# Kernel optimization log

Measured on AMD Instinct MI355X. Metric: run time of the kernel, lower is better.

Reference implementation:

```python
import jax, jax.numpy as jnp
from jax import lax
import numpy as np

DIM = 768
HEADS = 12
HD = DIM // HEADS  # 64
STRIDE = (1, 2, 2)
KER = (3, 3, 3)
PAD = [(1, 1), (1, 1), (1, 1)]
EPS = 1e-5


def _layernorm(x, g, b):
    mu = jnp.mean(x, axis=-1, keepdims=True)
    var = jnp.var(x, axis=-1, keepdims=True)
    return (x - mu) * lax.rsqrt(var + EPS) * g + b


def _attention_pool(t, wconv, g, b, T, H, W):
    # t: [B, heads, 1 + T*H*W, HD]; depthwise conv3d pooling on non-cls tokens
    B, Nh, _, Cd = t.shape
    cls_tok = t[:, :, :1, :]
    body = t[:, :, 1:, :].reshape(B * Nh, T, H, W, Cd).transpose(0, 4, 1, 2, 3)  # [BN, C, T, H, W]
    body = lax.conv_general_dilated(
        body, wconv, window_strides=STRIDE, padding=PAD,
        feature_group_count=Cd,
        dimension_numbers=('NCDHW', 'OIDHW', 'NCDHW'))
    Tp, Hp, Wp = body.shape[2], body.shape[3], body.shape[4]
    body = body.reshape(B, Nh, Cd, Tp * Hp * Wp).transpose(0, 1, 3, 2)  # [B, heads, Lp, C]
    t = jnp.concatenate([cls_tok, body], axis=2)
    t = _layernorm(t, g, b)
    return t, (Tp, Hp, Wp)


def setup_inputs() -> dict:
    key = jax.random.key(0)
    ks = jax.random.split(key, 12)
    T, H, W = 8, 28, 28
    B = 4
    N = 1 + T * H * W  # cls + thw tokens = 6273
    s = 0.02
    inp = {
        'x': jax.random.normal(ks[0], (B, N, DIM), jnp.float32),
        'qkv_w': jax.random.normal(ks[1], (DIM, 3 * DIM), jnp.float32) * s,
        'qkv_b': jnp.zeros((3 * DIM,), jnp.float32),
        'proj_w': jax.random.normal(ks[2], (DIM, DIM), jnp.float32) * s,
        'proj_b': jnp.zeros((DIM,), jnp.float32),
        'wq': jax.random.normal(ks[3], (HD, 1, 3, 3, 3), jnp.float32) * s,
        'wk': jax.random.normal(ks[4], (HD, 1, 3, 3, 3), jnp.float32) * s,
        'wv': jax.random.normal(ks[5], (HD, 1, 3, 3, 3), jnp.float32) * s,
        'gq': jnp.ones((HD,), jnp.float32), 'bq': jnp.zeros((HD,), jnp.float32),
        'gk': jnp.ones((HD,), jnp.float32), 'bk': jnp.zeros((HD,), jnp.float32),
        'gv': jnp.ones((HD,), jnp.float32), 'bv': jnp.zeros((HD,), jnp.float32),
        'thw_t': T, 'thw_h': H, 'thw_w': W,
    }
    return inp


def reference(x, qkv_w, qkv_b, proj_w, proj_b, wq, wk, wv,
              gq, bq, gk, bk, gv, bv, thw_t, thw_h, thw_w):
    B, N, C = x.shape
    scale = HD ** -0.5
    qkv = (x @ qkv_w + qkv_b).reshape(B, N, 3, HEADS, HD).transpose(2, 0, 3, 1, 4)
    q, k, v = qkv[0], qkv[1], qkv[2]  # [B, heads, N, HD]
    q, q_shape = _attention_pool(q, wq, gq, bq, thw_t, thw_h, thw_w)
    k, _ = _attention_pool(k, wk, gk, bk, thw_t, thw_h, thw_w)
    v, _ = _attention_pool(v, wv, gv, bv, thw_t, thw_h, thw_w)
    attn = jax.nn.softmax(jnp.einsum('bhqd,bhkd->bhqk', q, k) * scale, axis=-1)
    Nq = q.shape[2]
    out = jnp.einsum('bhqk,bhkd->bhqd', attn, v).transpose(0, 2, 1, 3).reshape(B, Nq, C)
    out = out @ proj_w + proj_b
    return out
```

## Files before the change

### kernel.cpp

```cpp
#include <hip/hip_runtime.h>
#include <hip/hip_bf16.h>

#define BB      4
#define NTOK    6273
#define NPOOL   1569
#define NPOOLP  1600
#define NHEADS  12
#define TT      8
#define HH      28
#define WW      28
#define HP      14
#define WP      14

typedef __attribute__((ext_vector_type(8))) _Float16 f16x8;
typedef __attribute__((ext_vector_type(4))) float f32x4;
typedef unsigned short u16;

#define AS1(p) ((const __attribute__((address_space(1))) void*)(p))
#define AS3(p) ((__attribute__((address_space(3))) void*)(p))

static __device__ __forceinline__ u16 f2h(float x) {
    union { _Float16 h; u16 u; } c; c.h = (_Float16)x; return c.u;
}
static __device__ __forceinline__ float h2f(u16 u) {
    union { u16 u; _Float16 h; } c; c.u = u; return (float)c.h;
}

__global__ __launch_bounds__(256) void cvt_f32_f16_kernel(
    const float* __restrict__ in, u16* __restrict__ out, int n4)
{
    int i = blockIdx.x * 256 + threadIdx.x;
    const int stride = gridDim.x * 256;
    for (; i < n4; i += stride) {
        const float4 v = ((const float4*)in)[i];
        ushort4 o;
        o.x = f2h(v.x); o.y = f2h(v.y); o.z = f2h(v.z); o.w = f2h(v.w);
        ((ushort4*)out)[i] = o;
    }
}

__global__ __launch_bounds__(256) void transpose_cvt_kernel(
    const float* __restrict__ W, u16* __restrict__ t, int K, int N)
{
    __shared__ float tile[32][33];
    const int n0 = blockIdx.x * 32, k0 = blockIdx.y * 32;
    const int tx = threadIdx.x, ty = threadIdx.y;
    #pragma unroll
    for (int i = 0; i < 4; ++i)
        tile[ty + i * 8][tx] = W[(size_t)(k0 + ty + i * 8) * N + n0 + tx];
    __syncthreads();
    #pragma unroll
    for (int i = 0; i < 4; ++i) {
        const int n = n0 + ty + i * 8;
        t[(size_t)n * K + k0 + tx] = f2h(tile[tx][ty + i * 8]);
    }
}

__global__ __launch_bounds__(256) void wt_transpose_kernel(
    const float* __restrict__ wq, const float* __restrict__ wk,
    const float* __restrict__ wv, u16* __restrict__ wTh)
{
    const int which = blockIdx.x;
    const float* w = (which == 0) ? wq : (which == 1) ? wk : wv;
    u16* o = wTh + which * 27 * 64;
    for (int i = threadIdx.x; i < 27 * 64; i += 256) {
        const int j = i >> 6, d = i & 63;
        o[j * 64 + d] = f2h(w[d * 27 + j]);
    }
}

#define GBK 64
#define GNKT 12

__global__ __launch_bounds__(512, 2) void gemm256_qkv_kernel(
    const u16* __restrict__ Af, const u16* __restrict__ Bt,
    const float* __restrict__ bias, int M,
    u16* __restrict__ o0, u16* __restrict__ o1, u16* __restrict__ o2)
{
    __shared__ __align__(16) u16 A_s[4][128 * 64];
    __shared__ __align__(16) u16 B_s[4][128 * 64];

    const int tid  = threadIdx.x;
    const int lane = tid & 63;
    const int w    = tid >> 6;
    const int wr   = w >> 2;
    const int wc   = w & 3;

    const int nwg = gridDim.x;
    const int qch = nwg >> 3, rch = nwg & 7;
    const int xcd = blockIdx.x & 7, idx = blockIdx.x >> 3;
    const int wg  = (xcd < rch ? xcd * (qch + 1) : rch * (qch + 1) + (xcd - rch) * qch) + idx;
    const int m0 = (wg / 9) * 256;
    const int nb = wg % 9;
    const int n0 = nb * 256;

    const int srow = tid >> 3;
    const int scc  = ((tid & 7) ^ (srow & 7)) * 8;
    unsigned offA[2][2], offB[2][2];
    #pragma unroll
    for (int h = 0; h < 2; ++h)
        #pragma unroll
        for (int i = 0; i < 2; ++i) {
            offA[h][i] = (unsigned)(min(m0 + h * 128 + i * 64 + srow, M - 1) * 768 + scc);
            offB[h][i] = (unsigned)((n0 + h * 128 + i * 64 + srow) * 768 + scc);
        }

#define STGA(slot, h, tt) do { \
    __builtin_amdgcn_global_load_lds(AS1(Af + offA[h][0] + (tt) * 64), AS3(&A_s[slot][w * 512]), 16, 0, 0); \
    __builtin_amdgcn_global_load_lds(AS1(Af + offA[h][1] + (tt) * 64), AS3(&A_s[slot][4096 + w * 512]), 16, 0, 0); \
} while (0)
#define STGB(slot, h, tt) do { \
    __builtin_amdgcn_global_load_lds(AS1(Bt + offB[h][0] + (tt) * 64), AS3(&B_s[slot][w * 512]), 16, 0, 0); \
    __builtin_amdgcn_global_load_lds(AS1(Bt + offB[h][1] + (tt) * 64), AS3(&B_s[slot][4096 + w * 512]), 16, 0, 0); \
} while (0)

    STGA(0, 0, 0); STGB(0, 0, 0); STGA(1, 1, 0); STGB(1, 1, 0);
    STGA(2, 0, 1); STGB(2, 0, 1); STGA(3, 1, 1);
    asm volatile("s_waitcnt vmcnt(6)" ::: "memory");
    __builtin_amdgcn_s_barrier();

    f32x4 acc[8][4] = {};
    const int fr = lane & 15, fq = lane >> 4;
    const int ck0 = (fq ^ (fr & 7)) * 8;
    const int ck1 = ((4 + fq) ^ (fr & 7)) * 8;
    const int arow = fr * 64;
    const int brow = (wc & 1) * 4096 + fr * 64;

    for (int it = 0; it < GNKT / 2; ++it) {
        #pragma unroll
        for (int par = 0; par < 2; ++par) {
            const int t  = it * 2 + par;
            const int sa = par ? 2 + wr : wr;
            const int sb = par ? 2 + (wc >> 1) : (wc >> 1);

            f16x8 aF[4][2], aG[4][2], bLo[2][2], bHi[2][2];

            if (t < GNKT - 1) STGB(par ? 1 : 3, 1, t + 1);
            #pragma unroll
            for (int m = 0; m < 4; ++m)
                #pragma unroll
                for (int kh = 0; kh < 2; ++kh)
                    aF[m][kh] = *(const f16x8*)&A_s[sa][m * 1024 + arow + (kh ? ck1 : ck0)];
            #pragma unroll
            for (int n = 0; n < 2; ++n)
                #pragma unroll
                for (int kh = 0; kh < 2; ++kh)
                    bLo[n][kh] = *(const f16x8*)&B_s[sb][brow + n * 1024 + (kh ? ck1 : ck0)];
            __builtin_amdgcn_s_setprio(1);
            #pragma unroll
            for (int m = 0; m < 4; ++m)
                #pragma unroll
                for (int n = 0; n < 2; ++n) {
                    acc[m][n] = __builtin_amdgcn_mfma_f32_16x16x32_f16(aF[m][0], bLo[n][0], acc[m][n], 0, 0, 0);
                    acc[m][n] = __builtin_amdgcn_mfma_f32_16x16x32_f16(aF[m][1], bLo[n][1], acc[m][n], 0, 0, 0);
                }
            __builtin_amdgcn_s_setprio(0);
            __builtin_amdgcn_s_barrier();

            #pragma unroll
            for (int n = 0; n < 2; ++n)
                #pragma unroll
                for (int kh = 0; kh < 2; ++kh)
                    bHi[n][kh] = *(const f16x8*)&B_s[sb][brow + (n + 2) * 1024 + (kh ? ck1 : ck0)];
            __builtin_amdgcn_s_setprio(1);
            #pragma unroll
            for (int m = 0; m < 4; ++m)
                #pragma unroll
                for (int n = 0; n < 2; ++n) {
                    acc[m][n + 2] = __builtin_amdgcn_mfma_f32_16x16x32_f16(aF[m][0], bHi[n][0], acc[m][n + 2], 0, 0, 0);
                    acc[m][n + 2] = __builtin_amdgcn_mfma_f32_16x16x32_f16(aF[m][1], bHi[n][1], acc[m][n + 2], 0, 0, 0);
                }
            __builtin_amdgcn_s_setprio(0);
            __builtin_amdgcn_s_barrier();

            if (t < GNKT - 2) STGB(par ? 2 : 0, 0, t + 2);
            #pragma unroll
            for (int m = 0; m < 4; ++m)
                #pragma unroll
                for (int kh = 0; kh < 2; ++kh)
                    aG[m][kh] = *(const f16x8*)&A_s[sa][(m + 4) * 1024 + arow + (kh ? ck1 : ck0)];
            __builtin_amdgcn_s_setprio(1);
            #pragma unroll
            for (int m = 0; m < 4; ++m)
                #pragma unroll
                for (int n = 0; n < 2; ++n) {
                    acc[m + 4][n + 2] = __builtin_amdgcn_mfma_f32_16x16x32_f16(aG[m][0], bHi[n][0], acc[m + 4][n + 2], 0, 0, 0);
                    acc[m + 4][n + 2] = __builtin_amdgcn_mfma_f32_16x16x32_f16(aG[m][1], bHi[n][1], acc[m + 4][n + 2], 0, 0, 0);
                }
            __builtin_amdgcn_s_setprio(0);
            __builtin_amdgcn_s_barrier();

            if (t < GNKT - 2) { STGA(par ? 2 : 0, 0, t + 2); STGA(par ? 3 : 1, 1, t + 2); }
            __builtin_amdgcn_s_setprio(1);
            #pragma unroll
            for (int m = 0; m < 4; ++m)
                #pragma unroll
                for (int n = 0; n < 2; ++n) {
                    acc[m + 4][n] = __builtin_amdgcn_mfma_f32_16x16x32_f16(aG[m][0], bLo[n][0], acc[m + 4][n], 0, 0, 0);
                    acc[m + 4][n] = __builtin_amdgcn_mfma_f32_16x16x32_f16(aG[m][1], bLo[n][1], acc[m + 4][n], 0, 0, 0);
                }
            __builtin_amdgcn_s_setprio(0);
            if (t < GNKT - 2) asm volatile("s_waitcnt vmcnt(6)" ::: "memory");
            else              asm volatile("s_waitcnt vmcnt(0)" ::: "memory");
            __builtin_amdgcn_s_barrier();
        }
    }
#undef STGA
#undef STGB

    const int s = nb / 3;
    u16* const dsts = (s == 0) ? o0 : (s == 1) ? o1 : o2;
    #pragma unroll
    for (int m = 0; m < 8; ++m) {
        const int growb = m0 + wr * 128 + m * 16 + fq * 4;
        #pragma unroll
        for (int j = 0; j < 4; ++j) {
            const int grow = growb + j;
            if (grow >= M) continue;
            const int bidx = grow / NTOK;
            const int ntok = grow - bidx * NTOK;
            #pragma unroll
            for (int n = 0; n < 4; ++n) {
                const int gcol = n0 + wc * 64 + n * 16 + fr;
                const float v = acc[m][n][j] + bias[gcol];
                const int rem = gcol - s * 768;
                const int h = rem >> 6, d = rem & 63;
                dsts[(size_t)((bidx * NHEADS + h) * NTOK + ntok) * 64 + d] = f2h(v);
            }
        }
    }
}

template<int NBLK, bool QKV, typename OutT>
__global__ __launch_bounds__(512) void gemm_fp16_kernel(
    const u16* __restrict__ Af, const u16* __restrict__ Bt,
    const float* __restrict__ bias, int M,
    OutT* __restrict__ o0, OutT* __restrict__ o1, OutT* __restrict__ o2)
{
    __shared__ __align__(16) u16 A_s[128 * 32];
    __shared__ __align__(16) u16 B_s[128 * 32];

    const int tid  = threadIdx.x;
    const int lane = tid & 63;
    const int w    = tid >> 6;
    const int wr   = w >> 2, wc = w & 3;

    const int nwg = gridDim.x;
    const int qch = nwg >> 3, rch = nwg & 7;
    const int xcd = blockIdx.x & 7, idx = blockIdx.x >> 3;
    const int wg  = (xcd < rch ? xcd * (qch + 1) : rch * (qch + 1) + (xcd - rch) * qch) + idx;
    const int m0 = (wg / NBLK) * 128;
    const int n0 = (wg % NBLK) * 128;

    f32x4 acc[4][2] = {};

    const int srow   = lane >> 2;
    const int sslot  = (lane & 3) ^ ((srow >> 1) & 3);

    for (int kt = 0; kt < 24; ++kt) {
        const int k0 = kt * 32;
        __syncthreads();

        {
            const int rb = w * 16;
            const int ra = min(m0 + rb + srow, M - 1);
            __builtin_amdgcn_global_load_lds(AS1(Af + (size_t)ra * 768 + k0 + sslot * 8),
                                             AS3(&A_s[rb * 32]), 16, 0, 0);
            __builtin_amdgcn_global_load_lds(AS1(Bt + (size_t)(n0 + rb + srow) * 768 + k0 + sslot * 8),
                                             AS3(&B_s[rb * 32]), 16, 0, 0);
        }
        __syncthreads();

        const int fr = lane & 15, fq = lane >> 4;
        const int rslot = (fq ^ ((fr >> 1) & 3)) << 3;
        f16x8 a[4], b[2];
        #pragma unroll
        for (int m = 0; m < 4; ++m)
            a[m] = *(const f16x8*)&A_s[(wr * 64 + m * 16 + fr) * 32 + rslot];
        #pragma unroll
        for (int n = 0; n < 2; ++n)
            b[n] = *(const f16x8*)&B_s[(wc * 32 + n * 16 + fr) * 32 + rslot];

        #pragma unroll
        for (int m = 0; m < 4; ++m)
            #pragma unroll
            for (int n = 0; n < 2; ++n)
                acc[m][n] = __builtin_amdgcn_mfma_f32_16x16x32_f16(a[m], b[n], acc[m][n], 0, 0, 0);
    }

    const int fr = lane & 15, fq = lane >> 4;
    #pragma unroll
    for (int m = 0; m < 4; ++m) {
        const int grow_base = m0 + wr * 64 + m * 16 + fq * 4;
        #pragma unroll
        for (int j = 0; j < 4; ++j) {
            const int grow = grow_base + j;
            if (grow >= M) continue;
            int b = 0, ntok = 0;
            if (QKV) { b = grow / NTOK; ntok = grow - b * NTOK; }
            #pragma unroll
            for (int n = 0; n < 2; ++n) {
                const int gcol = n0 + wc * 32 + n * 16 + fr;
                const float v = acc[m][n][j] + bias[gcol];
                if (QKV) {
                    const int s = gcol / 768;
                    const int rem = gcol - s * 768;
                    const int h = rem >> 6, d = rem & 63;
                    OutT* dst = (s == 0) ? o0 : (s == 1) ? o1 : o2;
                    dst[(size_t)((b * NHEADS + h) * NTOK + ntok) * 64 + d] = (OutT)f2h(v);
                } else {
                    o0[(size_t)grow * (NBLK * 128) + gcol] = (OutT)v;
                }
            }
        }
    }
}

#define PL_PG  50
#define PL_NWG (3 * 48 * PL_PG)
__global__ __launch_bounds__(256) void pool_ln_kernel(
    const u16* __restrict__ qr, const u16* __restrict__ kr, const u16* __restrict__ vr,
    const u16* __restrict__ wTh,
    const float* __restrict__ gq, const float* __restrict__ bq,
    const float* __restrict__ gk, const float* __restrict__ bk,
    const float* __restrict__ gv, const float* __restrict__ bv,
    u16* __restrict__ qph, u16* __restrict__ kph, u16* __restrict__ vpt)
{
    const int wg = (blockIdx.x & 7) * (PL_NWG / 8) + (blockIdx.x >> 3);
    const int which = wg / (48 * PL_PG);
    const int rem   = wg - which * (48 * PL_PG);
    const int bh    = rem / PL_PG;
    const int pg    = rem - bh * PL_PG;
    const int wv_   = threadIdx.x >> 6;
    const int lane  = threadIdx.x & 63;
    const int tg    = lane >> 3;
    const int d0    = (lane & 7) * 8;

    const int p  = pg * 32 + wv_ * 8 + tg;
    const int pc = min(p, NPOOL - 1);

    const u16*   in  = (which == 0) ? qr : (which == 1) ? kr : vr;
    const u16*   wTb = wTh + which * 27 * 64;
    const float* g   = (which == 0) ? gq : (which == 1) ? gk : gv;
    const float* bb_ = (which == 0) ? bq : (which == 1) ? bk : bv;
    const float qscale = (which == 0) ? 0.125f : 1.0f;

    const size_t inb = (size_t)bh * NTOK * 64;

    float s[8] = {};
    if (pc == 0) {
        const f16x8 t = *(const f16x8*)&in[inb + d0];
        #pragma unroll
        for (int c = 0; c < 8; ++c) s[c] = (float)t[c];
    } else {
        const int idx = pc - 1;
        const int tp = idx / (HP * WP);
        const int r2 = idx - tp * (HP * WP);
        const int hp = r2 / WP;
        const int wp = r2 - hp * WP;

        const f16x8 z8 = (f16x8)(_Float16)0.0f;
        #pragma unroll
        for (int kt = 0; kt < 3; ++kt) {
            const int it = tp + kt - 1;
            #pragma unroll
            for (int kh = 0; kh < 3; ++kh) {
                const int ih = hp * 2 + kh - 1;
                #pragma unroll
                for (int kw = 0; kw < 3; ++kw) {
                    const int iw = wp * 2 + kw - 1;
                    const int j  = kt * 9 + kh * 3 + kw;
                    const bool ok = (it >= 0) & (it < TT) & (ih >= 0) & (ih < HH) &
                                    (iw >= 0) & (iw < WW);
                    const int n   = 1 + (it * HH + ih) * WW + iw;
                    const int n_c = ok ? n : 0;
                    const f16x8 tv  = *(const f16x8*)&in[inb + (size_t)n_c * 64 + d0];
                    const f16x8 wv8 = *(const f16x8*)&wTb[j * 64 + d0];
                    const f16x8 ts  = ok ? tv : z8;
                    #pragma unroll
                    for (int c = 0; c < 8; ++c)
                        s[c] = fmaf((float)wv8[c], (float)ts[c], s[c]);
                }
            }
        }
    }

    float sum = 0.f, ssq = 0.f;
    #pragma unroll
    for (int c = 0; c < 8; ++c) { sum += s[c]; ssq += s[c] * s[c]; }
    #pragma unroll
    for (int off = 1; off < 8; off <<= 1) {
        sum += __shfl_xor(sum, off);
        ssq += __shfl_xor(ssq, off);
    }
    const float mu  = sum * (1.f / 64.f);
    const float var = ssq * (1.f / 64.f) - mu * mu;
    const float rs  = rsqrtf(var + 1e-5f);

    float g8[8], b8[8];
    {
        const float4 g0 = *(const float4*)&g[d0];
        const float4 g1 = *(const float4*)&g[d0 + 4];
        const float4 b0 = *(const float4*)&bb_[d0];
        const float4 b1 = *(const float4*)&bb_[d0 + 4];
        g8[0]=g0.x; g8[1]=g0.y; g8[2]=g0.z; g8[3]=g0.w;
        g8[4]=g1.x; g8[5]=g1.y; g8[6]=g1.z; g8[7]=g1.w;
        b8[0]=b0.x; b8[1]=b0.y; b8[2]=b0.z; b8[3]=b0.w;
        b8[4]=b1.x; b8[5]=b1.y; b8[6]=b1.z; b8[7]=b1.w;
    }

    u16 oo[8];
    #pragma unroll
    for (int c = 0; c < 8; ++c)
        oo[c] = f2h(((s[c] - mu) * rs * g8[c] + b8[c]) * qscale);

    if (which == 2) {
        u16* base = vpt + (size_t)bh * 64 * NPOOLP + p;
        if (p < NPOOL) {
            #pragma unroll
            for (int c = 0; c < 8; ++c)
                base[(size_t)(d0 + c) * NPOOLP] = oo[c];
        } else {
            #pragma unroll
            for (int c = 0; c < 8; ++c)
                base[(size_t)(d0 + c) * NPOOLP] = 0;
        }
    } else if (p < NPOOL) {
        u16* out = (which == 0) ? qph : kph;
        u16* dst = &out[((size_t)bh * NPOOL + p) * 64 + d0];
        *(ushort4*)&dst[0] = *(ushort4*)&oo[0];
        *(ushort4*)&dst[4] = *(ushort4*)&oo[4];
    }
}

__global__ __launch_bounds__(256) void flash_attn_fp16_kernel(
    const u16* __restrict__ qh, const u16* __restrict__ kh,
    const u16* __restrict__ vt, float* __restrict__ accf,
    float* __restrict__ lf)
{
    __shared__ __align__(16) u16 K_s[64 * 64];
    __shared__ __align__(16) u16 V_s[64 * 64];
    __shared__ __align__(16) u16 P_s[4][32 * 64];

    const int bh = blockIdx.y;
    const int q0 = blockIdx.x * 128;
    const int z  = blockIdx.z;
    const int kt_lo = z ? 13 : 0, kt_hi = z ? 25 : 13;
    const int tid = threadIdx.x;
    const int w = tid >> 6, lane = tid & 63;
    const int fr = lane & 15, fq = lane >> 4;
    const int l8 = lane >> 3;
    const int sw = 8 * ((lane & 7) ^ l8);

    const size_t hb  = (size_t)bh * NPOOL * 64;
    const size_t vtb = (size_t)bh * 64 * NPOOLP;
    float* accb = accf + (size_t)z * BB * NPOOL * 768;
    float* lb   = lf   + (size_t)z * 48 * NPOOL;

    f16x8 qf_[2][2];
    #pragma unroll
    for (int qf = 0; qf < 2; ++qf) {
        const int row = min(q0 + w * 32 + qf * 16 + fr, NPOOL - 1);
        #pragma unroll
        for (int half = 0; half < 2; ++half)
            qf_[qf][half] = *(const f16x8*)&qh[hb + (size_t)row * 64 + half * 32 + fq * 8];
    }

    f16x8 ones;
    #pragma unroll
    for (int i = 0; i < 8; ++i) ones[i] = (_Float16)1.0f;

    f32x4 acc[2][4] = {};
    f32x4 l_acc[2] = {};

    #define LDSW(buf, row, colbyte) \
        (*(const f16x8*)((const char*)(buf) + ((row) * 128 + ((colbyte) ^ (((row) & 7) << 4)))))

    for (int kt = kt_lo; kt < kt_hi; ++kt) {
        const int k0 = kt * 64;
        __syncthreads();

        #pragma unroll
        for (int i = 0; i < 2; ++i) {
            const int rb = w * 16 + i * 8;
            const int r  = rb + l8;
            const int gk = min(k0 + r, NPOOL - 1);
            __builtin_amdgcn_global_load_lds(AS1(kh + hb + (size_t)gk * 64 + sw),
                                             AS3(&K_s[rb * 64]), 16, 0, 0);
            __builtin_amdgcn_global_load_lds(AS1(vt + vtb + (size_t)r * NPOOLP + k0 + sw),
                                             AS3(&V_s[rb * 64]), 16, 0, 0);
        }
        __syncthreads();

        f32x4 sv[2][4];
        #pragma unroll
        for (int nf = 0; nf < 4; ++nf) {
            const int krow = nf * 16 + fr;
            const f16x8 kf0 = LDSW(K_s, krow, fq * 16);
            const f16x8 kf1 = LDSW(K_s, krow, 64 + fq * 16);
            #pragma unroll
            for (int qf = 0; qf < 2; ++qf) {
                f32x4 s = {};
                s = __builtin_amdgcn_mfma_f32_16x16x32_f16(qf_[qf][0], kf0, s, 0, 0, 0);
                s = __builtin_amdgcn_mfma_f32_16x16x32_f16(qf_[qf][1], kf1, s, 0, 0, 0);
                sv[qf][nf] = s;
            }
        }

        #pragma unroll
        for (int nf = 0; nf < 4; ++nf) {
            const bool valid = (k0 + nf * 16 + fr) < NPOOL;
            #pragma unroll
            for (int qf = 0; qf < 2; ++qf) {
                #pragma unroll
                for (int j = 0; j < 4; ++j) {
                    const float p = valid ? __expf(sv[qf][nf][j]) : 0.f;
                    const int row = qf * 16 + fq * 4 + j;
                    const int bo  = row * 128 + ((nf * 32 + fr * 2) ^ ((row & 7) << 4));
                    *(u16*)((char*)&P_s[w][0] + bo) = f2h(p);
                }
            }
        }
        __builtin_amdgcn_sched_barrier(0);

        f16x8 pa[2][2];
        #pragma unroll
        for (int qf = 0; qf < 2; ++qf) {
            const int prow = qf * 16 + fr;
            pa[qf][0] = LDSW(&P_s[w][0], prow, fq * 16);
            pa[qf][1] = LDSW(&P_s[w][0], prow, 64 + fq * 16);
            l_acc[qf] = __builtin_amdgcn_mfma_f32_16x16x32_f16(pa[qf][0], ones, l_acc[qf], 0, 0, 0);
            l_acc[qf] = __builtin_amdgcn_mfma_f32_16x16x32_f16(pa[qf][1], ones, l_acc[qf], 0, 0, 0);
        }
        #pragma unroll
        for (int df = 0; df < 4; ++df) {
            const int vrow = df * 16 + fr;
            const f16x8 v0 = LDSW(V_s, vrow, fq * 16);
            const f16x8 v1 = LDSW(V_s, vrow, 64 + fq * 16);
            acc[0][df] = __builtin_amdgcn_mfma_f32_16x16x32_f16(pa[0][0], v0, acc[0][df], 0, 0, 0);
            acc[0][df] = __builtin_amdgcn_mfma_f32_16x16x32_f16(pa[0][1], v1, acc[0][df], 0, 0, 0);
            acc[1][df] = __builtin_amdgcn_mfma_f32_16x16x32_f16(pa[1][0], v0, acc[1][df], 0, 0, 0);
            acc[1][df] = __builtin_amdgcn_mfma_f32_16x16x32_f16(pa[1][1], v1, acc[1][df], 0, 0, 0);
        }
    }
    #undef LDSW

    const int b = bh / NHEADS, h = bh % NHEADS;
    #pragma unroll
    for (int qf = 0; qf < 2; ++qf) {
        #pragma unroll
        for (int j = 0; j < 4; ++j) {
            const int q = q0 + w * 32 + qf * 16 + fq * 4 + j;
            if (q >= NPOOL) continue;
            float* dst = &accb[((size_t)b * NPOOL + q) * 768 + h * 64];
            #pragma unroll
            for (int df = 0; df < 4; ++df)
                dst[df * 16 + fr] = acc[qf][df][j];
            if (fr == 0)
                lb[(size_t)bh * NPOOL + q] = l_acc[qf][j];
        }
    }
}

__global__ __launch_bounds__(256) void combine_kernel(
    const float* __restrict__ acc0, const float* __restrict__ acc1,
    const float* __restrict__ l0, const float* __restrict__ l1,
    u16* __restrict__ aoh)
{
    const int n4 = BB * NPOOL * 768 / 4;
    int i = blockIdx.x * 256 + threadIdx.x;
    const int stride = gridDim.x * 256;
    for (; i < n4; i += stride) {
        const int e0  = i * 4;
        const int row = e0 / 768;
        const int c   = e0 - row * 768;
        const int b   = row / NPOOL;
        const int q   = row - b * NPOOL;
        const int h   = c >> 6;
        const size_t li = (size_t)(b * NHEADS + h) * NPOOL + q;
        const float inv = 1.f / (l0[li] + l1[li]);
        const float4 a0 = ((const float4*)acc0)[i];
        const float4 a1 = ((const float4*)acc1)[i];
        ushort4 o;
        o.x = f2h((a0.x + a1.x) * inv);
        o.y = f2h((a0.y + a1.y) * inv);
        o.z = f2h((a0.z + a1.z) * inv);
        o.w = f2h((a0.w + a1.w) * inv);
        ((ushort4*)aoh)[i] = o;
    }
}

extern "C" void kernel_launch(void* const* d_in, const int* in_sizes, int n_in,
                              void* d_out, int out_size, void* d_ws, size_t ws_size,
                              hipStream_t stream)
{
    const float* x      = (const float*)d_in[0];
    const float* qkv_w  = (const float*)d_in[1];
    const float* qkv_b  = (const float*)d_in[2];
    const float* proj_w = (const float*)d_in[3];
    const float* proj_b = (const float*)d_in[4];
    const float* wq     = (const float*)d_in[5];
    const float* wk     = (const float*)d_in[6];
    const float* wv     = (const float*)d_in[7];
    const float* gq     = (const float*)d_in[8];
    const float* bq     = (const float*)d_in[9];
    const float* gk     = (const float*)d_in[10];
    const float* bk     = (const float*)d_in[11];
    const float* gv     = (const float*)d_in[12];
    const float* bv     = (const float*)d_in[13];

    const size_t RAW  = (size_t)BB * NHEADS * NTOK * 64;
    const size_t PLD  = (size_t)BB * NHEADS * NPOOL * 64;
    const size_t VTSZ = (size_t)BB * NHEADS * 64 * NPOOLP;
    const size_t AOSZ = (size_t)BB * NPOOL * 768;

    u16* q_raw = (u16*)d_ws;
    u16* k_raw = q_raw + RAW;
    u16* v_raw = k_raw + RAW;
    u16* xh    = v_raw + RAW;
    u16* qph   = xh + RAW;
    u16* kph   = qph + PLD;
    u16* vpb   = kph + PLD;
    u16* vpt   = vpb + PLD;
    u16* wth   = vpt + VTSZ;
    u16* pwth  = wth + (size_t)2304 * 768;
    u16* wTh   = pwth + (size_t)768 * 768;
    float* acc0 = (float*)(wTh + 3 * 27 * 64);
    float* acc1 = acc0 + AOSZ;
    float* l0   = acc1 + AOSZ;
    float* l1   = l0 + (size_t)48 * NPOOL;
    u16* aoh   = q_raw;

    cvt_f32_f16_kernel<<<2048, 256, 0, stream>>>(x, xh, (int)(RAW / 4));

    transpose_cvt_kernel<<<dim3(2304 / 32, 768 / 32), dim3(32, 8), 0, stream>>>(
        qkv_w, wth, 768, 2304);
    transpose_cvt_kernel<<<dim3(768 / 32, 768 / 32), dim3(32, 8), 0, stream>>>(
        proj_w, pwth, 768, 768);
    wt_transpose_kernel<<<3, 256, 0, stream>>>(wq, wk, wv, wTh);

    gemm256_qkv_kernel<<<dim3(99 * 9), 512, 0, stream>>>(
        xh, wth, qkv_b, BB * NTOK, q_raw, k_raw, v_raw);

    pool_ln_kernel<<<dim3(PL_NWG), 256, 0, stream>>>(
        q_raw, k_raw, v_raw, wTh, gq, bq, gk, bk, gv, bv,
        qph, kph, vpt);

    flash_attn_fp16_kernel<<<dim3(13, 48, 2), 256, 0, stream>>>(
        qph, kph, vpt, acc0, l0);

    combine_kernel<<<2048, 256, 0, stream>>>(acc0, acc1, l0, l1, aoh);

    gemm_fp16_kernel<6, false, float><<<dim3(50 * 6), 512, 0, stream>>>(
        aoh, pwth, proj_b, BB * NPOOL, (float*)d_out, nullptr, nullptr);
}
```

Before: 319.9 us.

## Restructure QKV GEMM main loop into register-prefetched double-buffered pipeline

Rewrites the K-loop of the QKV projection GEMM. Each iteration now stages a full A/B tile pair two steps ahead, and the next tile's A-low and B-low fragments are prefetched into registers during the current tile's last MFMA phases. Fragment loads are interleaved with MFMA groups, and the B global offsets are folded into a single base plus constants to save registers. The intent is to hide LDS read latency and simplify the load schedule. The cost is a stricter vmcnt(0) wait each iteration and higher register pressure from the persistent fragment registers.

After: 311.2 us. -2.7%, faster.

```diff
diff --git a/kernel.cpp b/kernel.cpp
--- a/kernel.cpp
+++ b/kernel.cpp
@@ -96,117 +96,140 @@
 
     const int srow = tid >> 3;
     const int scc  = ((tid & 7) ^ (srow & 7)) * 8;
-    unsigned offA[2][2], offB[2][2];
+    unsigned offA[2][2];
     #pragma unroll
     for (int h = 0; h < 2; ++h)
         #pragma unroll
-        for (int i = 0; i < 2; ++i) {
+        for (int i = 0; i < 2; ++i)
             offA[h][i] = (unsigned)(min(m0 + h * 128 + i * 64 + srow, M - 1) * 768 + scc);
-            offB[h][i] = (unsigned)((n0 + h * 128 + i * 64 + srow) * 768 + scc);
-        }
+    const unsigned offB0 = (unsigned)((n0 + srow) * 768 + scc);
 
 #define STGA(slot, h, tt) do { \
     __builtin_amdgcn_global_load_lds(AS1(Af + offA[h][0] + (tt) * 64), AS3(&A_s[slot][w * 512]), 16, 0, 0); \
     __builtin_amdgcn_global_load_lds(AS1(Af + offA[h][1] + (tt) * 64), AS3(&A_s[slot][4096 + w * 512]), 16, 0, 0); \
 } while (0)
 #define STGB(slot, h, tt) do { \
-    __builtin_amdgcn_global_load_lds(AS1(Bt + offB[h][0] + (tt) * 64), AS3(&B_s[slot][w * 512]), 16, 0, 0); \
-    __builtin_amdgcn_global_load_lds(AS1(Bt + offB[h][1] + (tt) * 64), AS3(&B_s[slot][4096 + w * 512]), 16, 0, 0); \
+    __builtin_amdgcn_global_load_lds(AS1(Bt + offB0 + (h) * 98304 + (tt) * 64), AS3(&B_s[slot][w * 512]), 16, 0, 0); \
+    __builtin_amdgcn_global_load_lds(AS1(Bt + offB0 + (h) * 98304 + 49152 + (tt) * 64), AS3(&B_s[slot][4096 + w * 512]), 16, 0, 0); \
 } while (0)
-
-    STGA(0, 0, 0); STGB(0, 0, 0); STGA(1, 1, 0); STGB(1, 1, 0);
-    STGA(2, 0, 1); STGB(2, 0, 1); STGA(3, 1, 1);
-    asm volatile("s_waitcnt vmcnt(6)" ::: "memory");
-    __builtin_amdgcn_s_barrier();
-
-    f32x4 acc[8][4] = {};
+#define STAGE(pair, tt) do { \
+    STGA((pair) * 2 + 0, 0, tt); STGA((pair) * 2 + 1, 1, tt); \
+    STGB((pair) * 2 + 0, 0, tt); STGB((pair) * 2 + 1, 1, tt); \
+} while (0)
+
     const int fr = lane & 15, fq = lane >> 4;
     const int ck0 = (fq ^ (fr & 7)) * 8;
     const int ck1 = ((4 + fq) ^ (fr & 7)) * 8;
     const int arow = fr * 64;
     const int brow = (wc & 1) * 4096 + fr * 64;
 
-    for (int it = 0; it < GNKT / 2; ++it) {
-        #pragma unroll
-        for (int par = 0; par < 2; ++par) {
-            const int t  = it * 2 + par;
-            const int sa = par ? 2 + wr : wr;
-            const int sb = par ? 2 + (wc >> 1) : (wc >> 1);
-
-            f16x8 aF[4][2], aG[4][2], bLo[2][2], bHi[2][2];
-
-            if (t < GNKT - 1) STGB(par ? 1 : 3, 1, t + 1);
-            #pragma unroll
-            for (int m = 0; m < 4; ++m)
-                #pragma unroll
-                for (int kh = 0; kh < 2; ++kh)
-                    aF[m][kh] = *(const f16x8*)&A_s[sa][m * 1024 + arow + (kh ? ck1 : ck0)];
-            #pragma unroll
-            for (int n = 0; n < 2; ++n)
-                #pragma unroll
-                for (int kh = 0; kh < 2; ++kh)
-                    bLo[n][kh] = *(const f16x8*)&B_s[sb][brow + n * 1024 + (kh ? ck1 : ck0)];
-            __builtin_amdgcn_s_setprio(1);
-            #pragma unroll
-            for (int m = 0; m < 4; ++m)
-                #pragma unroll
-                for (int n = 0; n < 2; ++n) {
-                    acc[m][n] = __builtin_amdgcn_mfma_f32_16x16x32_f16(aF[m][0], bLo[n][0], acc[m][n], 0, 0, 0);
-                    acc[m][n] = __builtin_amdgcn_mfma_f32_16x16x32_f16(aF[m][1], bLo[n][1], acc[m][n], 0, 0, 0);
-                }
-            __builtin_amdgcn_s_setprio(0);
-            __builtin_amdgcn_s_barrier();
-
-            #pragma unroll
-            for (int n = 0; n < 2; ++n)
-                #pragma unroll
-                for (int kh = 0; kh < 2; ++kh)
-                    bHi[n][kh] = *(const f16x8*)&B_s[sb][brow + (n + 2) * 1024 + (kh ? ck1 : ck0)];
-            __builtin_amdgcn_s_setprio(1);
-            #pragma unroll
-            for (int m = 0; m < 4; ++m)
-                #pragma unroll
-                for (int n = 0; n < 2; ++n) {
-                    acc[m][n + 2] = __builtin_amdgcn_mfma_f32_16x16x32_f16(aF[m][0], bHi[n][0], acc[m][n + 2], 0, 0, 0);
-                    acc[m][n + 2] = __builtin_amdgcn_mfma_f32_16x16x32_f16(aF[m][1], bHi[n][1], acc[m][n + 2], 0, 0, 0);
-                }
-            __builtin_amdgcn_s_setprio(0);
-            __builtin_amdgcn_s_barrier();
-
-            if (t < GNKT - 2) STGB(par ? 2 : 0, 0, t + 2);
-            #pragma unroll
-            for (int m = 0; m < 4; ++m)
-                #pragma unroll
-                for (int kh = 0; kh < 2; ++kh)
-                    aG[m][kh] = *(const f16x8*)&A_s[sa][(m + 4) * 1024 + arow + (kh ? ck1 : ck0)];
-            __builtin_amdgcn_s_setprio(1);
-            #pragma unroll
-            for (int m = 0; m < 4; ++m)
-                #pragma unroll
-                for (int n = 0; n < 2; ++n) {
-                    acc[m + 4][n + 2] = __builtin_amdgcn_mfma_f32_16x16x32_f16(aG[m][0], bHi[n][0], acc[m + 4][n + 2], 0, 0, 0);
-                    acc[m + 4][n + 2] = __builtin_amdgcn_mfma_f32_16x16x32_f16(aG[m][1], bHi[n][1], acc[m + 4][n + 2], 0, 0, 0);
-                }
-            __builtin_amdgcn_s_setprio(0);
-            __builtin_amdgcn_s_barrier();
-
-            if (t < GNKT - 2) { STGA(par ? 2 : 0, 0, t + 2); STGA(par ? 3 : 1, 1, t + 2); }
-            __builtin_amdgcn_s_setprio(1);
-            #pragma unroll
-            for (int m = 0; m < 4; ++m)
-                #pragma unroll
-                for (int n = 0; n < 2; ++n) {
-                    acc[m + 4][n] = __builtin_amdgcn_mfma_f32_16x16x32_f16(aG[m][0], bLo[n][0], acc[m + 4][n], 0, 0, 0);
-                    acc[m + 4][n] = __builtin_amdgcn_mfma_f32_16x16x32_f16(aG[m][1], bLo[n][1], acc[m + 4][n], 0, 0, 0);
-                }
-            __builtin_amdgcn_s_setprio(0);
-            if (t < GNKT - 2) asm volatile("s_waitcnt vmcnt(6)" ::: "memory");
-            else              asm volatile("s_waitcnt vmcnt(0)" ::: "memory");
-            __builtin_amdgcn_s_barrier();
-        }
+    f32x4 acc[8][4] = {};
+    f16x8 aLo[4][2], aHi[4][2], bLo[2][2], bHi[2][2];
+
+    STAGE(0, 0);
+    STAGE(1, 1);
+    asm volatile("s_waitcnt vmcnt(8)" ::: "memory");
+    __builtin_amdgcn_s_barrier();
+    {
+        const u16* As = &A_s[wr][0];
+        const u16* Bs = &B_s[wc >> 1][0];
+        #pragma unroll
+        for (int m = 0; m < 4; ++m) {
+            aLo[m][0] = *(const f16x8*)&As[m * 1024 + arow + ck0];
+            aLo[m][1] = *(const f16x8*)&As[m * 1024 + arow + ck1];
+        }
+        #pragma unroll
+        for (int n = 0; n < 2; ++n) {
+            bLo[n][0] = *(const f16x8*)&Bs[brow + n * 1024 + ck0];
+            bLo[n][1] = *(const f16x8*)&Bs[brow + n * 1024 + ck1];
+        }
+    }
+
+    for (int t = 0; t < GNKT; ++t) {
+        const int pair = t & 1;
+        const u16* As  = &A_s[pair * 2 + wr][0];
+        const u16* Bs  = &B_s[pair * 2 + (wc >> 1)][0];
+        const u16* AsN = &A_s[(pair ^ 1) * 2 + wr][0];
+        const u16* BsN = &B_s[(pair ^ 1) * 2 + (wc >> 1)][0];
+
+        #pragma unroll
+        for (int m = 0; m < 2; ++m) {
+            aHi[m][0] = *(const f16x8*)&As[(m + 4) * 1024 + arow + ck0];
+            aHi[m][1] = *(const f16x8*)&As[(m + 4) * 1024 + arow + ck1];
+        }
+        #pragma unroll
+        for (int n = 0; n < 2; ++n) {
+            bHi[n][0] = *(const f16x8*)&Bs[brow + (n + 2) * 1024 + ck0];
+            bHi[n][1] = *(const f16x8*)&Bs[brow + (n + 2) * 1024 + ck1];
+        }
+        __builtin_amdgcn_s_setprio(1);
+        #pragma unroll
+        for (int m = 0; m < 4; ++m)
+            #pragma unroll
+            for (int n = 0; n < 2; ++n) {
+                acc[m][n] = __builtin_amdgcn_mfma_f32_16x16x32_f16(aLo[m][0], bLo[n][0], acc[m][n], 0, 0, 0);
+                acc[m][n] = __builtin_amdgcn_mfma_f32_16x16x32_f16(aLo[m][1], bLo[n][1], acc[m][n], 0, 0, 0);
+            }
+        __builtin_amdgcn_s_setprio(0);
+        __builtin_amdgcn_s_barrier();
+
+        #pragma unroll
+        for (int m = 2; m < 4; ++m) {
+            aHi[m][0] = *(const f16x8*)&As[(m + 4) * 1024 + arow + ck0];
+            aHi[m][1] = *(const f16x8*)&As[(m + 4) * 1024 + arow + ck1];
+        }
+        __builtin_amdgcn_s_setprio(1);
+        #pragma unroll
+        for (int m = 0; m < 4; ++m)
+            #pragma unroll
+            for (int n = 0; n < 2; ++n) {
+                acc[m][n + 2] = __builtin_amdgcn_mfma_f32_16x16x32_f16(aLo[m][0], bHi[n][0], acc[m][n + 2], 0, 0, 0);
+                acc[m][n + 2] = __builtin_amdgcn_mfma_f32_16x16x32_f16(aLo[m][1], bHi[n][1], acc[m][n + 2], 0, 0, 0);
+            }
+        __builtin_amdgcn_s_setprio(0);
+        asm volatile("s_waitcnt vmcnt(0)" ::: "memory");
+        __builtin_amdgcn_s_barrier();
+
+        if (t < GNKT - 2) STAGE(pair, t + 2);
+        __builtin_amdgcn_s_setprio(1);
+        #pragma unroll
+        for (int m = 0; m < 4; ++m)
+            #pragma unroll
+            for (int n = 0; n < 2; ++n) {
+                acc[m + 4][n + 2] = __builtin_amdgcn_mfma_f32_16x16x32_f16(aHi[m][0], bHi[n][0], acc[m + 4][n + 2], 0, 0, 0);
+                acc[m + 4][n + 2] = __builtin_amdgcn_mfma_f32_16x16x32_f16(aHi[m][1], bHi[n][1], acc[m + 4][n + 2], 0, 0, 0);
+            }
+        __builtin_amdgcn_s_setprio(0);
+        __builtin_amdgcn_s_barrier();
+
+        if (t < GNKT - 1) {
+            #pragma unroll
+            for (int m = 0; m < 4; ++m) {
+                aLo[m][0] = *(const f16x8*)&AsN[m * 1024 + arow + ck0];
+                aLo[m][1] = *(const f16x8*)&AsN[m * 1024 + arow + ck1];
+            }
+        }
+        __builtin_amdgcn_s_setprio(1);
+        #pragma unroll
+        for (int m = 0; m < 4; ++m)
+            #pragma unroll
+            for (int n = 0; n < 2; ++n) {
+                acc[m + 4][n] = __builtin_amdgcn_mfma_f32_16x16x32_f16(aHi[m][0], bLo[n][0], acc[m + 4][n], 0, 0, 0);
+                acc[m + 4][n] = __builtin_amdgcn_mfma_f32_16x16x32_f16(aHi[m][1], bLo[n][1], acc[m + 4][n], 0, 0, 0);
+            }
+        __builtin_amdgcn_s_setprio(0);
+        if (t < GNKT - 1) {
+            #pragma unroll
+            for (int n = 0; n < 2; ++n) {
+                bLo[n][0] = *(const f16x8*)&BsN[brow + n * 1024 + ck0];
+                bLo[n][1] = *(const f16x8*)&BsN[brow + n * 1024 + ck1];
+            }
+        }
+        __builtin_amdgcn_s_barrier();
     }
 #undef STGA
 #undef STGB
+#undef STAGE
 
     const int s = nb / 3;
     u16* const dsts = (s == 0) ? o0 : (s == 1) ? o1 : o2;
```
